# Performance work log

Hardware: AMD Instinct MI355X
Metric: run time of the kernel (lower is better)

The kernel has to match this reference:

```python
import jax, jax.numpy as jnp
import numpy as np

N = 100000
E = 1600000
IN_C = 256
OUT_C = 64


def setup_inputs() -> dict:
    key = jax.random.key(0)
    k1, k2, k3, k4, k5 = jax.random.split(key, 5)
    x = jax.random.normal(k1, (N, IN_C), dtype=jnp.float32)
    edge_index = jax.random.randint(k2, (2, E), 0, N, dtype=jnp.int64)
    edge_weight = jax.random.uniform(k3, (E,), dtype=jnp.float32)
    # GCNConv linear weight (Glorot-style scale) and bias
    W = jax.random.normal(k4, (IN_C, OUT_C), dtype=jnp.float32) * (1.0 / np.sqrt(IN_C))
    b = jax.random.normal(k5, (OUT_C,), dtype=jnp.float32) * 0.01
    return {"x": x, "edge_index": edge_index, "edge_weight": edge_weight, "W": W, "b": b}


def reference(x, edge_index, edge_weight, W, b):
    n = x.shape[0]
    row, col = edge_index[0], edge_index[1]  # source -> target (PyG source_to_target flow)
    # add self-loops with weight 1.0 (GCNConv default add_self_loops=True)
    loop = jnp.arange(n, dtype=edge_index.dtype)
    row = jnp.concatenate([row, loop])
    col = jnp.concatenate([col, loop])
    ew = jnp.concatenate([edge_weight, jnp.ones((n,), dtype=x.dtype)])
    # symmetric normalization: deg computed on target nodes
    deg = jax.ops.segment_sum(ew, col, num_segments=n)
    dinv = jnp.where(deg > 0, jax.lax.rsqrt(deg), 0.0)
    norm = dinv[row] * ew * dinv[col]  # [E+N]
    # dense linear transform first (fewer FLOPs than transforming per-edge)
    h = x @ W  # [N, OUT_C]
    # gather messages from source, scale, scatter-add to target
    out = jax.ops.segment_sum(norm[:, None] * h[row], col, num_segments=n)
    out = out + b
    # activation is None -> module returns (val, ()); we return val
    return out
```

## Files before the change

### kernel.cpp

```cpp
#include <hip/hip_runtime.h>
#include <hip/hip_fp16.h>


#define BS 256
#define EPB 4096
#define BSH 8
#define MAXB 8192

typedef unsigned long long u64;
typedef unsigned int u32;
typedef unsigned short u16;
typedef unsigned char u8;

typedef __attribute__((ext_vector_type(8))) short bf16x8;
typedef __attribute__((ext_vector_type(4))) float f32x4;

__device__ inline u16 f2bf(float f) {
    u32 u = __float_as_uint(f);
    return (u16)((u + 0x7fffu + ((u >> 16) & 1u)) >> 16);
}
__device__ inline u32 pack2bf(float a, float b) {
    return (u32)f2bf(a) | ((u32)f2bf(b) << 16);
}

__global__ __launch_bounds__(BS) void k_hist(const int* __restrict__ col,
                                             u32* __restrict__ cursor,
                                             u32* __restrict__ blockbase,
                                             int nbuck, int nblk, int e) {
    __shared__ u32 c1[512];
    int tid = threadIdx.x;
    for (int t = tid; t < nbuck; t += BS) c1[t] = 0;
    __syncthreads();
    int base = blockIdx.x * EPB;
#pragma unroll
    for (int j = 0; j < 16; ++j) {
        int i = base + j * BS + tid;
        if (i < e) atomicAdd(&c1[col[i] >> BSH], 1u);
    }
    __syncthreads();
    for (int t = tid; t < nbuck; t += BS) {
        u32 v = c1[t];
        if (v) blockbase[(size_t)t * nblk + blockIdx.x] = atomicAdd(&cursor[t], v);
    }
}

__global__ __launch_bounds__(512) void k_scan(const u32* __restrict__ cursor,
                                              u32* __restrict__ bstart, int nbuck) {
    __shared__ u32 s[512];
    int tid = threadIdx.x;
    u32 v = (tid < nbuck) ? cursor[tid] : 0;
    s[tid] = v;
    __syncthreads();
    for (int off = 1; off < 512; off <<= 1) {
        u32 t = (tid >= off) ? s[tid - off] : 0;
        __syncthreads();
        s[tid] += t;
        __syncthreads();
    }
    if (tid < nbuck) bstart[tid] = s[tid] - v;
    if (tid == nbuck - 1) bstart[nbuck] = s[tid];
}

#define GBM2 128
#define XAP 40

__global__ __launch_bounds__(BS) void k_g3(const float* __restrict__ x,
                                           const float* __restrict__ W,
                                           u16* __restrict__ hh, int n, int ngemm,
                                           const int* __restrict__ row,
                                           const int* __restrict__ col,
                                           const float* __restrict__ ew,
                                           const u32* __restrict__ bstart,
                                           const u32* __restrict__ blockbase,
                                           u64* __restrict__ pack,
                                           int nbuck, int nblk, int e) {
    __shared__ __align__(16) u16 xa[GBM2 * XAP];
    __shared__ __align__(16) u16 wt[64 * XAP];
    __shared__ u32 comb[512];
    __shared__ u32 rnk[512];
    const int tid = threadIdx.x;

    if ((int)blockIdx.x >= ngemm) {
        int blk = blockIdx.x - ngemm;
        for (int t = tid; t < nbuck; t += BS) {
            comb[t] = bstart[t] + blockbase[(size_t)t * nblk + blk];
            rnk[t] = 0;
        }
        __syncthreads();
        int base = blk * EPB;
#pragma unroll
        for (int j = 0; j < 16; ++j) {
            int i = base + j * BS + tid;
            if (i < e) {
                int c = col[i];
                int b = c >> BSH;
                u32 r = atomicAdd(&rnk[b], 1u);
                u32 pos = comb[b] + r;
                __half eh = __float2half(ew[i]);
                u64 en = (u64)(u32)row[i]
                       | ((u64)(u32)(c & 255) << 32)
                       | ((u64)(u16)__half_as_ushort(eh) << 48);
                pack[pos] = en;
            }
        }
        return;
    }
    const int lane = tid & 63;
    const int wid  = tid >> 6;
    const int lr = lane & 15;
    const int lg = lane >> 4;
    const int rb = blockIdx.x * GBM2;
    const int wrow = wid * 32;

    f32x4 acc[2][4];
#pragma unroll
    for (int rt = 0; rt < 2; ++rt)
#pragma unroll
        for (int ct = 0; ct < 4; ++ct) acc[rt][ct] = (f32x4){0.f, 0.f, 0.f, 0.f};

    const int srow = tid >> 1;
    const int skh  = (tid & 1) * 16;
    const int wc   = tid >> 2;
    const int wk   = (tid & 3) * 8;

    for (int kc = 0; kc < 256; kc += 32) {
        {
            int gr = rb + srow; if (gr >= n) gr = n - 1;
            const float4* src = reinterpret_cast<const float4*>(&x[(size_t)gr * 256 + kc + skh]);
            float4 a0 = src[0], a1 = src[1], a2 = src[2], a3 = src[3];
            uint4 v0, v1;
            v0.x = pack2bf(a0.x, a0.y); v0.y = pack2bf(a0.z, a0.w);
            v0.z = pack2bf(a1.x, a1.y); v0.w = pack2bf(a1.z, a1.w);
            v1.x = pack2bf(a2.x, a2.y); v1.y = pack2bf(a2.z, a2.w);
            v1.z = pack2bf(a3.x, a3.y); v1.w = pack2bf(a3.z, a3.w);
            *reinterpret_cast<uint4*>(&xa[srow * XAP + skh]) = v0;
            *reinterpret_cast<uint4*>(&xa[srow * XAP + skh + 8]) = v1;
        }
        {
            float w0 = W[(size_t)(kc + wk + 0) * 64 + wc];
            float w1 = W[(size_t)(kc + wk + 1) * 64 + wc];
            float w2 = W[(size_t)(kc + wk + 2) * 64 + wc];
            float w3 = W[(size_t)(kc + wk + 3) * 64 + wc];
            float w4 = W[(size_t)(kc + wk + 4) * 64 + wc];
            float w5 = W[(size_t)(kc + wk + 5) * 64 + wc];
            float w6 = W[(size_t)(kc + wk + 6) * 64 + wc];
            float w7 = W[(size_t)(kc + wk + 7) * 64 + wc];
            u32* dst = reinterpret_cast<u32*>(&wt[wc * XAP + wk]);
            dst[0] = pack2bf(w0, w1);
            dst[1] = pack2bf(w2, w3);
            dst[2] = pack2bf(w4, w5);
            dst[3] = pack2bf(w6, w7);
        }
        __syncthreads();

        bf16x8 af0 = *reinterpret_cast<const bf16x8*>(&xa[(wrow + lr) * XAP + lg * 8]);
        bf16x8 af1 = *reinterpret_cast<const bf16x8*>(&xa[(wrow + 16 + lr) * XAP + lg * 8]);
#pragma unroll
        for (int ct = 0; ct < 4; ++ct) {
            bf16x8 bfr = *reinterpret_cast<const bf16x8*>(&wt[(ct * 16 + lr) * XAP + lg * 8]);
            acc[0][ct] = __builtin_amdgcn_mfma_f32_16x16x32_bf16(af0, bfr, acc[0][ct], 0, 0, 0);
            acc[1][ct] = __builtin_amdgcn_mfma_f32_16x16x32_bf16(af1, bfr, acc[1][ct], 0, 0, 0);
        }
        __syncthreads();
    }

#pragma unroll
    for (int rt = 0; rt < 2; ++rt) {
        int grow0 = rb + wrow + rt * 16 + lg * 4;
#pragma unroll
        for (int reg = 0; reg < 4; ++reg) {
            int grow = grow0 + reg;
            if (grow < n) {
#pragma unroll
                for (int ct = 0; ct < 4; ++ct) {
                    hh[(size_t)grow * 64 + ct * 16 + lr] =
                        __half_as_ushort(__float2half(acc[rt][ct][reg]));
                }
            }
        }
    }
}

__global__ __launch_bounds__(512) void k_b2(const u32* __restrict__ bstart,
                                            u64* __restrict__ pack,
                                            float* __restrict__ dinv,
                                            int* __restrict__ offs,
                                            int n, int nbuck) {
    __shared__ u32 lrow[MAXB];
    __shared__ u16 lew[MAXB];
    __shared__ u8  lcl[MAXB];
    __shared__ u32 cnt[256];
    __shared__ float wdeg[256];
    __shared__ u32 pos[256];
    __shared__ float ldsd[256];
    int b = blockIdx.x;
    int tid = threadIdx.x;
    u32 gbase = bstart[b];
    int size = (int)(bstart[b + 1] - gbase);
    if (size > MAXB) size = MAXB;
    if (tid < 256) { cnt[tid] = 0; wdeg[tid] = 0.0f; }
    __syncthreads();
    for (int j = tid; j < size; j += 512) {
        u64 en = pack[gbase + j];
        u32 r = (u32)en;
        u32 cl = (u32)(en >> 32) & 255u;
        u16 eh = (u16)(en >> 48);
        lrow[j] = r;
        lcl[j] = (u8)cl;
        lew[j] = eh;
        atomicAdd(&cnt[cl], 1u);
        atomicAdd(&wdeg[cl], __half2float(__ushort_as_half(eh)));
    }
    __syncthreads();
    u32 myc = (tid < 256) ? cnt[tid] : 0;
    for (int off = 1; off < 256; off <<= 1) {
        u32 t = 0;
        if (tid < 256 && tid >= (u32)off) t = cnt[tid - off];
        __syncthreads();
        if (tid < 256) cnt[tid] += t;
        __syncthreads();
    }
    if (tid < 256) {
        u32 st = cnt[tid] - myc;
        pos[tid] = st;
        float dv = rsqrtf(1.0f + wdeg[tid]);
        ldsd[tid] = dv;
        int c = (b << BSH) + tid;
        if (c < n) {
            dinv[c] = dv;
            offs[c] = (int)(gbase + st);
        }
    }
    __syncthreads();
    for (int j = tid; j < size; j += 512) {
        u32 cl = lcl[j];
        u32 r = atomicAdd(&pos[cl], 1u);
        float w = __half2float(__ushort_as_half(lew[j])) * ldsd[cl];
        pack[gbase + r] = ((u64)__float_as_uint(w) << 32) | (u64)lrow[j];
    }
}

__global__ __launch_bounds__(BS) void k_reduce(const u64* __restrict__ sorted,
                                               const int* __restrict__ offs,
                                               const float* __restrict__ dinv,
                                               const __half2* __restrict__ hh,
                                               const float* __restrict__ bias,
                                               float* __restrict__ out, int n, int e) {
    int node = blockIdx.x * 4 + (threadIdx.x >> 6);
    int lane = threadIdx.x & 63;
    if (node >= n) return;
    int cc  = lane & 31;
    int ehi = lane >> 5;
    int s = offs[node];
    int t = (node + 1 < n) ? offs[node + 1] : e;
    float ax = 0.0f, ay = 0.0f;
    int j = s;
    for (; j + 7 < t; j += 8) {
        u64 p0 = sorted[j     + ehi];
        u64 p1 = sorted[j + 2 + ehi];
        u64 p2 = sorted[j + 4 + ehi];
        u64 p3 = sorted[j + 6 + ehi];
        int r0 = (int)(u32)p0, r1 = (int)(u32)p1, r2 = (int)(u32)p2, r3 = (int)(u32)p3;
        float n0 = __uint_as_float((u32)(p0 >> 32)) * dinv[r0];
        float n1 = __uint_as_float((u32)(p1 >> 32)) * dinv[r1];
        float n2 = __uint_as_float((u32)(p2 >> 32)) * dinv[r2];
        float n3 = __uint_as_float((u32)(p3 >> 32)) * dinv[r3];
        float2 f0 = __half22float2(hh[(size_t)r0 * 32 + cc]);
        float2 f1 = __half22float2(hh[(size_t)r1 * 32 + cc]);
        float2 f2 = __half22float2(hh[(size_t)r2 * 32 + cc]);
        float2 f3 = __half22float2(hh[(size_t)r3 * 32 + cc]);
        ax += n0 * f0.x; ay += n0 * f0.y;
        ax += n1 * f1.x; ay += n1 * f1.y;
        ax += n2 * f2.x; ay += n2 * f2.y;
        ax += n3 * f3.x; ay += n3 * f3.y;
    }
    for (; j + 1 < t; j += 2) {
        u64 p = sorted[j + ehi];
        int r = (int)(u32)p;
        float nn = __uint_as_float((u32)(p >> 32)) * dinv[r];
        float2 f = __half22float2(hh[(size_t)r * 32 + cc]);
        ax += nn * f.x; ay += nn * f.y;
    }
    if (j < t && ehi == 0) {
        u64 p = sorted[j];
        int r = (int)(u32)p;
        float nn = __uint_as_float((u32)(p >> 32)) * dinv[r];
        float2 f = __half22float2(hh[(size_t)r * 32 + cc]);
        ax += nn * f.x; ay += nn * f.y;
    }
    ax += __shfl_xor(ax, 32);
    ay += __shfl_xor(ay, 32);
    if (ehi == 0) {
        float di = dinv[node];
        float2 fs = __half22float2(hh[(size_t)node * 32 + cc]);
        float2 bb = *reinterpret_cast<const float2*>(&bias[cc * 2]);
        float2 r;
        r.x = ax + di * di * fs.x + bb.x;
        r.y = ay + di * di * fs.y + bb.y;
        reinterpret_cast<float2*>(out)[(size_t)node * 32 + cc] = r;
    }
}

__global__ __launch_bounds__(BS) void k_init_f(float* __restrict__ deg, int n) {
    int i = blockIdx.x * BS + threadIdx.x;
    if (i < n) deg[i] = 1.0f;
}
__global__ __launch_bounds__(BS) void k_count_f(const int* __restrict__ col,
                                                const float* __restrict__ ew,
                                                float* __restrict__ deg, int e) {
    int i = blockIdx.x * BS + threadIdx.x;
    if (i < e) unsafeAtomicAdd(&deg[col[i]], ew[i]);
}
__global__ __launch_bounds__(BS) void k_dinv_f(float* __restrict__ deg, int n) {
    int i = blockIdx.x * BS + threadIdx.x;
    if (i < n) {
        float d = deg[i];
        deg[i] = d > 0.0f ? rsqrtf(d) : 0.0f;
    }
}
__global__ __launch_bounds__(BS) void k_gemm_f(const float* __restrict__ x,
                                               const float* __restrict__ W,
                                               float* __restrict__ h, int n) {
    __shared__ float xsh[4 * 256];
    int b0 = blockIdx.x * 4;
    const float4* xv = reinterpret_cast<const float4*>(x + (size_t)b0 * 256);
    reinterpret_cast<float4*>(xsh)[threadIdx.x] = xv[threadIdx.x];
    __syncthreads();
    int rl = threadIdx.x >> 6;
    int c  = threadIdx.x & 63;
    const float* xr = xsh + rl * 256;
    float acc = 0.0f;
#pragma unroll 8
    for (int k = 0; k < 256; ++k) acc += xr[k] * W[k * 64 + c];
    int r = b0 + rl;
    if (r < n) h[(size_t)r * 64 + c] = acc;
}
__global__ __launch_bounds__(BS) void k_out_init(const float* __restrict__ h,
                                                 const float* __restrict__ dinv,
                                                 const float* __restrict__ bias,
                                                 float* __restrict__ out, int n64) {
    int i = blockIdx.x * BS + threadIdx.x;
    if (i < n64) {
        int r = i >> 6, c = i & 63;
        float di = dinv[r];
        out[i] = bias[c] + di * di * h[i];
    }
}
__global__ __launch_bounds__(BS) void k_scatter(const int* __restrict__ row,
                                                const int* __restrict__ col,
                                                const float* __restrict__ ew,
                                                const float* __restrict__ dinv,
                                                const float* __restrict__ h,
                                                float* __restrict__ out, int e) {
    int idx = blockIdx.x * BS + threadIdx.x;
    int ei = idx >> 6;
    int c  = idx & 63;
    if (ei >= e) return;
    int r = row[ei];
    int t = col[ei];
    float nrm = dinv[r] * ew[ei] * dinv[t];
    unsafeAtomicAdd(&out[(size_t)t * 64 + c], nrm * h[(size_t)r * 64 + c]);
}

extern "C" void kernel_launch(void* const* d_in, const int* in_sizes, int n_in,
                              void* d_out, int out_size, void* d_ws, size_t ws_size,
                              hipStream_t stream) {
    const float* x   = (const float*)d_in[0];
    const int*   ei  = (const int*)d_in[1];
    const float* ew  = (const float*)d_in[2];
    const float* W   = (const float*)d_in[3];
    const float* b   = (const float*)d_in[4];
    float* out = (float*)d_out;

    const int n = in_sizes[0] / 256;
    const int e = in_sizes[1] / 2;
    const int* row = ei;
    const int* col = ei + e;
    const int nbuck = (n + 255) >> 8;
    const int nblk  = (e + EPB - 1) / EPB;
    const int ngemm = (n + GBM2 - 1) / GBM2;

    size_t off = 0;
    auto alloc = [&](size_t elems) { size_t p = off; off += (elems + 63) & ~63ull; return p; };
    size_t o_cursor = alloc(nbuck);
    size_t o_bstart = alloc(nbuck + 1);
    size_t o_bbase  = alloc((size_t)nbuck * nblk);
    size_t o_pack   = alloc((size_t)e * 2);
    size_t o_offs   = alloc(n);
    size_t o_dinv   = alloc(n);
    size_t o_h      = alloc((size_t)n * 32);
    size_t needed = off * 4;

    u32*   wsu = (u32*)d_ws;
    float* wsf = (float*)d_ws;
    int*   wsi = (int*)d_ws;

    if (ws_size >= needed) {
        u32*   cursor = wsu + o_cursor;
        u32*   bstart = wsu + o_bstart;
        u32*   bbase  = wsu + o_bbase;
        u64*   pack   = (u64*)(wsu + o_pack);
        int*   offs   = wsi + o_offs;
        float* dinv   = wsf + o_dinv;
        u16*   hh     = (u16*)(wsu + o_h);

        hipMemsetAsync(cursor, 0, (size_t)nbuck * 4, stream);
        k_hist<<<nblk, BS, 0, stream>>>(col, cursor, bbase, nbuck, nblk, e);
        k_scan<<<1, 512, 0, stream>>>(cursor, bstart, nbuck);
        k_g3<<<ngemm + nblk, BS, 0, stream>>>(x, W, hh, n, ngemm,
                                              row, col, ew, bstart, bbase, pack,
                                              nbuck, nblk, e);
        k_b2<<<nbuck, 512, 0, stream>>>(bstart, pack, dinv, offs, n, nbuck);
        k_reduce<<<(n + 3) / 4, BS, 0, stream>>>(pack, offs, dinv,
                                                 (const __half2*)hh, b, out, n, e);
    } else {
        float* deg = wsf;
        float* h   = wsf + ((n + 63) & ~63);
        const int nb = (n + BS - 1) / BS;
        const int eb = (e + BS - 1) / BS;
        k_init_f<<<nb, BS, 0, stream>>>(deg, n);
        k_count_f<<<eb, BS, 0, stream>>>(col, ew, deg, e);
        k_dinv_f<<<nb, BS, 0, stream>>>(deg, n);
        k_gemm_f<<<(n + 3) / 4, BS, 0, stream>>>(x, W, h, n);
        k_out_init<<<((n * 64) + BS - 1) / BS, BS, 0, stream>>>(h, deg, b, out, n * 64);
        k_scatter<<<((size_t)e * 64 + BS - 1) / BS, BS, 0, stream>>>(row, col, ew, deg, h, out, e);
    }
}
```

Measured before the change: 145.5 us.

## Replace histogram+scan bucketing with fixed-capacity buckets and block-local sort

Result: faster. 129.6 us (-10.9%).

```diff
diff --git a/kernel.cpp b/kernel.cpp
--- a/kernel.cpp
+++ b/kernel.cpp
@@ -3,9 +3,9 @@
 
 
 #define BS 256
-#define EPB 4096
+#define EPB2 2048
 #define BSH 8
-#define MAXB 8192
+#define CAP 4608
 
 typedef unsigned long long u64;
 typedef unsigned int u32;
@@ -23,88 +23,87 @@
     return (u32)f2bf(a) | ((u32)f2bf(b) << 16);
 }
 
-__global__ __launch_bounds__(BS) void k_hist(const int* __restrict__ col,
-                                             u32* __restrict__ cursor,
-                                             u32* __restrict__ blockbase,
-                                             int nbuck, int nblk, int e) {
-    __shared__ u32 c1[512];
-    int tid = threadIdx.x;
-    for (int t = tid; t < nbuck; t += BS) c1[t] = 0;
-    __syncthreads();
-    int base = blockIdx.x * EPB;
-#pragma unroll
-    for (int j = 0; j < 16; ++j) {
-        int i = base + j * BS + tid;
-        if (i < e) atomicAdd(&c1[col[i] >> BSH], 1u);
-    }
-    __syncthreads();
-    for (int t = tid; t < nbuck; t += BS) {
-        u32 v = c1[t];
-        if (v) blockbase[(size_t)t * nblk + blockIdx.x] = atomicAdd(&cursor[t], v);
-    }
-}
-
-__global__ __launch_bounds__(512) void k_scan(const u32* __restrict__ cursor,
-                                              u32* __restrict__ bstart, int nbuck) {
-    __shared__ u32 s[512];
-    int tid = threadIdx.x;
-    u32 v = (tid < nbuck) ? cursor[tid] : 0;
-    s[tid] = v;
-    __syncthreads();
-    for (int off = 1; off < 512; off <<= 1) {
-        u32 t = (tid >= off) ? s[tid - off] : 0;
-        __syncthreads();
-        s[tid] += t;
-        __syncthreads();
-    }
-    if (tid < nbuck) bstart[tid] = s[tid] - v;
-    if (tid == nbuck - 1) bstart[nbuck] = s[tid];
-}
-
 #define GBM2 128
 #define XAP 40
 
-__global__ __launch_bounds__(BS) void k_g3(const float* __restrict__ x,
+__global__ __launch_bounds__(BS) void k_g4(const float* __restrict__ x,
                                            const float* __restrict__ W,
                                            u16* __restrict__ hh, int n, int ngemm,
                                            const int* __restrict__ row,
                                            const int* __restrict__ col,
                                            const float* __restrict__ ew,
-                                           const u32* __restrict__ bstart,
-                                           const u32* __restrict__ blockbase,
+                                           u32* __restrict__ cursor,
                                            u64* __restrict__ pack,
-                                           int nbuck, int nblk, int e) {
-    __shared__ __align__(16) u16 xa[GBM2 * XAP];
-    __shared__ __align__(16) u16 wt[64 * XAP];
-    __shared__ u32 comb[512];
-    __shared__ u32 rnk[512];
+                                           int nbuck, int e) {
+    __shared__ __align__(16) u8 smem[32768];
     const int tid = threadIdx.x;
 
     if ((int)blockIdx.x >= ngemm) {
+        u64* ent  = (u64*)smem;
+        u16* bkt  = (u16*)(smem + 16384);
+        u16* sidx = (u16*)(smem + 20480);
+        u32* cnt  = (u32*)(smem + 24576);
+        u32* scn  = (u32*)(smem + 26624);
+        u32* lpos = (u32*)(smem + 28672);
+        u32* gb   = (u32*)(smem + 30720);
         int blk = blockIdx.x - ngemm;
-        for (int t = tid; t < nbuck; t += BS) {
-            comb[t] = bstart[t] + blockbase[(size_t)t * nblk + blk];
-            rnk[t] = 0;
-        }
-        __syncthreads();
-        int base = blk * EPB;
-#pragma unroll
-        for (int j = 0; j < 16; ++j) {
-            int i = base + j * BS + tid;
-            if (i < e) {
+        int base = blk * EPB2;
+        int ej = e - base; if (ej > EPB2) ej = EPB2;
+
+        cnt[tid] = 0; cnt[tid + 256] = 0;
+        __syncthreads();
+#pragma unroll
+        for (int j = 0; j < 8; ++j) {
+            int lj = j * BS + tid;
+            if (lj < ej) {
+                int i = base + lj;
                 int c = col[i];
                 int b = c >> BSH;
-                u32 r = atomicAdd(&rnk[b], 1u);
-                u32 pos = comb[b] + r;
                 __half eh = __float2half(ew[i]);
-                u64 en = (u64)(u32)row[i]
-                       | ((u64)(u32)(c & 255) << 32)
-                       | ((u64)(u16)__half_as_ushort(eh) << 48);
-                pack[pos] = en;
+                ent[lj] = (u64)(u32)row[i]
+                        | ((u64)(u32)(c & 255) << 32)
+                        | ((u64)(u16)__half_as_ushort(eh) << 48);
+                bkt[lj] = (u16)b;
+                atomicAdd(&cnt[b], 1u);
             }
         }
+        __syncthreads();
+        scn[tid] = cnt[tid];
+        scn[tid + 256] = cnt[tid + 256];
+        __syncthreads();
+        for (int off = 1; off < 512; off <<= 1) {
+            u32 a0 = (tid >= off) ? scn[tid - off] : 0u;
+            u32 a1 = scn[tid + 256 - off];
+            __syncthreads();
+            scn[tid] += a0;
+            scn[tid + 256] += a1;
+            __syncthreads();
+        }
+        for (int t = tid; t < 512; t += 256) {
+            u32 c = cnt[t];
+            lpos[t] = scn[t] - c;
+            if (c) gb[t] = atomicAdd(&cursor[t], c);
+        }
+        __syncthreads();
+#pragma unroll
+        for (int j = 0; j < 8; ++j) {
+            int lj = j * BS + tid;
+            if (lj < ej) {
+                u32 p = atomicAdd(&lpos[bkt[lj]], 1u);
+                sidx[p] = (u16)lj;
+            }
+        }
+        __syncthreads();
+        for (int p = tid; p < ej; p += 256) {
+            int lj = sidx[p];
+            int b = bkt[lj];
+            u32 local = (u32)p - (scn[b] - cnt[b]) + gb[b];
+            if (local < CAP) pack[(size_t)b * CAP + local] = ent[lj];
+        }
         return;
     }
+    u16* xa = (u16*)smem;
+    u16* wt = (u16*)(smem + 10240);
     const int lane = tid & 63;
     const int wid  = tid >> 6;
     const int lr = lane & 15;
@@ -181,10 +180,12 @@
     }
 }
 
-__global__ __launch_bounds__(512) void k_b2(const u32* __restrict__ bstart,
+#define MAXB CAP
+__global__ __launch_bounds__(512) void k_b2(const u32* __restrict__ cursor,
                                             u64* __restrict__ pack,
                                             float* __restrict__ dinv,
                                             int* __restrict__ offs,
+                                            int* __restrict__ ends,
                                             int n, int nbuck) {
     __shared__ u32 lrow[MAXB];
     __shared__ u16 lew[MAXB];
@@ -195,8 +196,8 @@
     __shared__ float ldsd[256];
     int b = blockIdx.x;
     int tid = threadIdx.x;
-    u32 gbase = bstart[b];
-    int size = (int)(bstart[b + 1] - gbase);
+    size_t gbase = (size_t)b * CAP;
+    int size = (int)cursor[b];
     if (size > MAXB) size = MAXB;
     if (tid < 256) { cnt[tid] = 0; wdeg[tid] = 0.0f; }
     __syncthreads();
@@ -229,6 +230,7 @@
         if (c < n) {
             dinv[c] = dv;
             offs[c] = (int)(gbase + st);
+            ends[c] = (int)(gbase + st + myc);
         }
     }
     __syncthreads();
@@ -242,17 +244,18 @@
 
 __global__ __launch_bounds__(BS) void k_reduce(const u64* __restrict__ sorted,
                                                const int* __restrict__ offs,
+                                               const int* __restrict__ ends,
                                                const float* __restrict__ dinv,
                                                const __half2* __restrict__ hh,
                                                const float* __restrict__ bias,
-                                               float* __restrict__ out, int n, int e) {
+                                               float* __restrict__ out, int n) {
     int node = blockIdx.x * 4 + (threadIdx.x >> 6);
     int lane = threadIdx.x & 63;
     if (node >= n) return;
     int cc  = lane & 31;
     int ehi = lane >> 5;
     int s = offs[node];
-    int t = (node + 1 < n) ? offs[node + 1] : e;
+    int t = ends[node];
     float ax = 0.0f, ay = 0.0f;
     int j = s;
     for (; j + 7 < t; j += 8) {
@@ -377,16 +380,15 @@
     const int* row = ei;
     const int* col = ei + e;
     const int nbuck = (n + 255) >> 8;
-    const int nblk  = (e + EPB - 1) / EPB;
+    const int nblk2 = (e + EPB2 - 1) / EPB2;
     const int ngemm = (n + GBM2 - 1) / GBM2;
 
     size_t off = 0;
     auto alloc = [&](size_t elems) { size_t p = off; off += (elems + 63) & ~63ull; return p; };
     size_t o_cursor = alloc(nbuck);
-    size_t o_bstart = alloc(nbuck + 1);
-    size_t o_bbase  = alloc((size_t)nbuck * nblk);
-    size_t o_pack   = alloc((size_t)e * 2);
+    size_t o_pack   = alloc((size_t)nbuck * CAP * 2);
     size_t o_offs   = alloc(n);
+    size_t o_ends   = alloc(n);
     size_t o_dinv   = alloc(n);
     size_t o_h      = alloc((size_t)n * 32);
     size_t needed = off * 4;
@@ -397,22 +399,19 @@
 
     if (ws_size >= needed) {
         u32*   cursor = wsu + o_cursor;
-        u32*   bstart = wsu + o_bstart;
-        u32*   bbase  = wsu + o_bbase;
         u64*   pack   = (u64*)(wsu + o_pack);
         int*   offs   = wsi + o_offs;
+        int*   ends   = wsi + o_ends;
         float* dinv   = wsf + o_dinv;
         u16*   hh     = (u16*)(wsu + o_h);
 
         hipMemsetAsync(cursor, 0, (size_t)nbuck * 4, stream);
-        k_hist<<<nblk, BS, 0, stream>>>(col, cursor, bbase, nbuck, nblk, e);
-        k_scan<<<1, 512, 0, stream>>>(cursor, bstart, nbuck);
-        k_g3<<<ngemm + nblk, BS, 0, stream>>>(x, W, hh, n, ngemm,
-                                              row, col, ew, bstart, bbase, pack,
-                                              nbuck, nblk, e);
-        k_b2<<<nbuck, 512, 0, stream>>>(bstart, pack, dinv, offs, n, nbuck);
-        k_reduce<<<(n + 3) / 4, BS, 0, stream>>>(pack, offs, dinv,
-                                                 (const __half2*)hh, b, out, n, e);
+        k_g4<<<ngemm + nblk2, BS, 0, stream>>>(x, W, hh, n, ngemm,
+                                               row, col, ew, cursor, pack,
+                                               nbuck, e);
+        k_b2<<<nbuck, 512, 0, stream>>>(cursor, pack, dinv, offs, ends, n, nbuck);
+        k_reduce<<<(n + 3) / 4, BS, 0, stream>>>(pack, offs, ends, dinv,
+                                                 (const __half2*)hh, b, out, n);
     } else {
         float* deg = wsf;
         float* h   = wsf + ((n + 63) & ~63);
```
